# Kernel optimization log

Hardware: AMD Instinct MI355X
Metric: run time of the kernel (lower is better)

Reference implementation:

```python
import jax, jax.numpy as jnp
import numpy as np

VOCAB, EMB = 5000, 300
UNITS = [256, 512, 256]  # two return_sequences layers + final return-last layer
DENSE = 64


def lstm_layer(x, W, U, b, return_seq):
    """Keras-style LSTM with activation='relu', recurrent_activation='sigmoid'.
    x: [B,T,D]; W: [D,4u]; U: [u,4u]; b: [4u]. Gate order: i, f, c, o."""
    B = x.shape[0]
    u = U.shape[0]
    xg = jnp.einsum('btd,dg->btg', x, W) + b  # precompute input projections [B,T,4u]

    def step(carry, xg_t):
        h, c = carry
        g = xg_t + h @ U
        i, f, cc, o = jnp.split(g, 4, axis=-1)
        i = jax.nn.sigmoid(i)
        f = jax.nn.sigmoid(f)
        o = jax.nn.sigmoid(o)
        c = f * c + i * jax.nn.relu(cc)
        h = o * jax.nn.relu(c)
        return (h, c), h

    h0 = jnp.zeros((B, u), x.dtype)
    (hT, _), hs = jax.lax.scan(step, (h0, h0), jnp.swapaxes(xg, 0, 1))
    return jnp.swapaxes(hs, 0, 1) if return_seq else hT


def setup_inputs() -> dict:
    key = jax.random.key(0)
    ks = iter(jax.random.split(key, 16))
    s = 0.05  # small init keeps relu-LSTM numerically stable
    inp = {
        'tokens': jax.random.randint(next(ks), (128, 512), 0, VOCAB, dtype=jnp.int32),
        'emb': jax.random.normal(next(ks), (VOCAB, EMB), jnp.float32) * s,
    }
    d = EMB
    for li, u in enumerate(UNITS):
        inp[f'W{li}'] = jax.random.normal(next(ks), (d, 4 * u), jnp.float32) * s
        inp[f'U{li}'] = jax.random.normal(next(ks), (u, 4 * u), jnp.float32) * s
        inp[f'b{li}'] = jnp.zeros((4 * u,), jnp.float32)
        d = u
    inp['Wd'] = jax.random.normal(next(ks), (UNITS[-1], DENSE), jnp.float32) * s
    inp['bd'] = jnp.zeros((DENSE,), jnp.float32)
    inp['Wc'] = jax.random.normal(next(ks), (DENSE, 1), jnp.float32) * s
    inp['bc'] = jnp.zeros((1,), jnp.float32)
    return inp


def reference(tokens, emb, W0, U0, b0, W1, U1, b1, W2, U2, b2, Wd, bd, Wc, bc):
    x = emb[tokens]                                   # [B,T,300]
    x = lstm_layer(x, W0, U0, b0, return_seq=True)    # [B,T,256]
    x = lstm_layer(x, W1, U1, b1, return_seq=True)    # [B,T,512]
    x = lstm_layer(x, W2, U2, b2, return_seq=False)   # [B,256]
    x = jax.nn.relu(x @ Wd + bd)                      # [B,64]
    return jax.nn.sigmoid(x @ Wc + bc)                # [B,1]
```

## Files before the change

### kernel.cpp

```cpp
#include <hip/hip_runtime.h>
#include <cstdint>
#include <cstddef>

#define BATCH  128
#define SEQT   512
#define EMB_D  300
#define VOCABN 5000
#define KP0    320
#define NU0    256
#define NU1    512
#define NU2    256
#define NDENSE 64
#define RING   32
#define LIM    (1 << 19)

typedef unsigned short ushortT;
typedef unsigned long long ull;
typedef __attribute__((ext_vector_type(8))) short bf16x8;
typedef __attribute__((ext_vector_type(8))) unsigned short u16x8;
typedef __attribute__((ext_vector_type(4))) unsigned short u16x4;
typedef __attribute__((ext_vector_type(4))) float f32x4;

#define AGT __HIP_MEMORY_SCOPE_AGENT

static __device__ __forceinline__ unsigned short f2bf(float x) {
    union { float f; unsigned u; } v; v.f = x;
    const unsigned r = v.u + 0x7FFFu + ((v.u >> 16) & 1u);
    return (unsigned short)(r >> 16);
}
static __device__ __forceinline__ float bf2f(unsigned short b) {
    union { unsigned u; float f; } v; v.u = ((unsigned)b) << 16;
    return v.f;
}
static __device__ __forceinline__ float sigmoidf_(float x) {
    return 1.f / (1.f + __expf(-x));
}
static __device__ __forceinline__ unsigned ald(const unsigned* p) {
    return __hip_atomic_load((unsigned*)p, __ATOMIC_RELAXED, AGT);
}
static __device__ __forceinline__ void ast(unsigned* p, unsigned v) {
    __hip_atomic_store(p, v, __ATOMIC_RELAXED, AGT);
}
static __device__ __forceinline__ void ld16c(u16x8* d, const void* p) {
    asm volatile("global_load_dwordx4 %0, %1, off sc0 sc1"
                 : "=&v"(*d) : "v"(p) : "memory");
}
static __device__ __forceinline__ void ld8c(u16x4* d, const void* p) {
    asm volatile("global_load_dwordx2 %0, %1, off sc0 sc1"
                 : "=&v"(*d) : "v"(p) : "memory");
}
static __device__ __forceinline__ void st4c(void* p, unsigned v) {
    asm volatile("global_store_dword %0, %1, off sc0 sc1"
                 :: "v"(p), "v"(v) : "memory");
}
static __device__ __forceinline__ void wait0() {
    asm volatile("s_waitcnt vmcnt(0)" ::: "memory");
    __builtin_amdgcn_sched_barrier(0);
}
static __device__ __forceinline__ void wait2() {
    asm volatile("s_waitcnt vmcnt(2)" ::: "memory");
    __builtin_amdgcn_sched_barrier(0);
}

__global__ __launch_bounds__(256) void convert_WT(
    const float* __restrict__ W, ushortT* __restrict__ WbfT,
    int K, int NG, int KP, int total)
{
    for (int idx = blockIdx.x * 256 + threadIdx.x; idx < total; idx += gridDim.x * 256) {
        const int m = idx / KP, k = idx - m * KP;
        WbfT[idx] = (k < K) ? f2bf(W[(size_t)k * NG + m]) : (ushortT)0;
    }
}
__global__ __launch_bounds__(256) void convert_emb(
    const float* __restrict__ emb, ushortT* __restrict__ embbf)
{
    const int total = VOCABN * KP0;
    for (int idx = blockIdx.x * 256 + threadIdx.x; idx < total; idx += gridDim.x * 256) {
        const int v = idx / KP0, k = idx - v * KP0;
        embbf[idx] = (k < EMB_D) ? f2bf(emb[(size_t)v * EMB_D + k]) : (ushortT)0;
    }
}

__global__ __launch_bounds__(256) void gemm_xg0(
    const ushortT* __restrict__ embbf,
    const int*   __restrict__ tokens,
    const ushortT* __restrict__ W0T,
    const float* __restrict__ bias,
    ushortT* __restrict__ xg0)
{
    __shared__ ushortT Wl[128][32];
    __shared__ ushortT Xl[128][32];
    __shared__ int tokL[128];

    const int tid = threadIdx.x;
    const int t   = blockIdx.x;
    const int m0  = blockIdx.y * 128;
    const int wv  = tid >> 6;
    const int lane = tid & 63;
    const int lo  = lane & 15;
    const int hi  = lane >> 4;

    if (tid < 128) tokL[tid] = tokens[tid * SEQT + t];
    __syncthreads();

    f32x4 acc[2][8];
    #pragma unroll
    for (int s = 0; s < 2; ++s)
        #pragma unroll
        for (int n = 0; n < 8; ++n)
            acc[s][n] = f32x4{0.f, 0.f, 0.f, 0.f};

    for (int k0 = 0; k0 < KP0; k0 += 32) {
        #pragma unroll
        for (int it = 0; it < 2; ++it) {
            const int idx = tid + it * 256;
            const int row = idx >> 2, gq = idx & 3;
            const int gs  = gq ^ ((row >> 1) & 3);
            *(u16x8*)&Wl[row][gs * 8] =
                *(const u16x8*)(W0T + (size_t)(m0 + row) * KP0 + k0 + gq * 8);
            *(u16x8*)&Xl[row][gs * 8] =
                *(const u16x8*)(embbf + (size_t)tokL[row] * KP0 + k0 + gq * 8);
        }
        __syncthreads();

        bf16x8 bfr[8];
        #pragma unroll
        for (int n = 0; n < 8; ++n) {
            const int row = n * 16 + lo;
            bfr[n] = *(const bf16x8*)&Xl[row][(hi ^ ((row >> 1) & 3)) * 8];
        }
        #pragma unroll
        for (int s = 0; s < 2; ++s) {
            const int row = wv * 32 + s * 16 + lo;
            const bf16x8 a = *(const bf16x8*)&Wl[row][(hi ^ ((row >> 1) & 3)) * 8];
            #pragma unroll
            for (int n = 0; n < 8; ++n)
                acc[s][n] = __builtin_amdgcn_mfma_f32_16x16x32_bf16(a, bfr[n], acc[s][n], 0, 0, 0);
        }
        __syncthreads();
    }

    #pragma unroll
    for (int s = 0; s < 2; ++s)
        #pragma unroll
        for (int j = 0; j < 4; ++j) {
            const int m = m0 + wv * 32 + s * 16 + hi * 4 + j;
            const float bi = bias[m];
            #pragma unroll
            for (int n = 0; n < 8; ++n)
                xg0[(((size_t)t * 8 + n) * 1024 + m) * 16 + lo] = f2bf(acc[s][n][j] + bi);
        }
}

template<int U_, bool XATOMIC, int XTSH, int XPH>
__device__ void rec_role(
    int rid,
    const float* __restrict__ Umat,
    const ushortT* __restrict__ xgring, int xmask,
    ushortT* __restrict__ hring,
    unsigned* Fown,
    unsigned* Xown,
    unsigned* Xguard, int nGd,
    char* smem)
{
    constexpr int NGu = 4 * U_;
    constexpr int WPG = U_ / 64;
    constexpr int NWF = WPG * 4;
    constexpr int KT  = U_ / 32;
    constexpr int GR  = U_ / 8;
    constexpr int NLD = (16 * GR) / 256;

    ushortT* hstage = (ushortT*)smem;

    const int tid = threadIdx.x, w = tid >> 6, lane = tid & 63;
    const int lo = lane & 15, hi = lane >> 4;
    const int grp = rid & 7, wgj = rid >> 3;
    const int b0 = grp * 16, J = wgj * 64;
    const int jcol = J + w * 16 + lo;
    const size_t S = (size_t)128 * U_;

    bf16x8 bfr[4][KT];
    #pragma unroll
    for (int g = 0; g < 4; ++g)
        #pragma unroll
        for (int kt = 0; kt < KT; ++kt) {
            const float* up = Umat + (size_t)(kt * 32 + hi * 8) * NGu + g * U_ + jcol;
            bf16x8 v;
            #pragma unroll
            for (int i = 0; i < 8; ++i) v[i] = (short)f2bf(up[(size_t)i * NGu]);
            bfr[g][kt] = v;
        }

    float creg[4] = {0.f, 0.f, 0.f, 0.f};

    if (XATOMIC) {
        if (w == 0) {
            int guard = 0; bool ok;
            do {
                bool pred = true;
                if (lane < 4) {
                    const int mt = (lane * U_ + J) >> XTSH;
                    pred = ((int)ald(&Xown[(mt * XPH) * 16]) >= 1);
                }
                ok = __all(pred);
                if (!ok) __builtin_amdgcn_s_sleep(2);
            } while (!ok && ++guard < LIM);
        }
        __syncthreads();
    }
    u16x4 xnext[4];
    {
        const size_t xb = (size_t)grp * NGu;
        #pragma unroll
        for (int g = 0; g < 4; ++g) {
            const ushortT* ap = xgring + (xb + g * U_ + jcol) * 16 + hi * 4;
            if (XATOMIC) ld8c(&xnext[g], ap);
            else         xnext[g] = *(const u16x4*)ap;
        }
        if (XATOMIC) wait0();
    }

    for (int t = 0; t < SEQT; ++t) {
        if (w == 0) {
            int guard = 0; bool ok;
            do {
                bool pred = true;
                if (t > 0 && lane < NWF)
                    pred = ((int)ald(&Fown[(grp * NWF + lane) * 16]) >= t);
                if (XATOMIC && t + 1 < SEQT && lane >= 40 && lane < 44) {
                    const int mt = ((lane - 40) * U_ + J) >> XTSH;
                    const int fi = mt * XPH + ((t + 1) & (XPH - 1));
                    pred = pred && ((int)ald(&Xown[fi * 16]) >= t + 2);
                }
                for (int i = lane; i < nGd; i += 64)
                    pred = pred && ((int)ald(&Xguard[i * 16]) >= t - (RING - 1));
                ok = __all(pred);
                if (!ok) __builtin_amdgcn_s_sleep(1);
            } while (!ok && ++guard < LIM);
        }
        __syncthreads();

        u16x4 xcur[4];
        #pragma unroll
        for (int g = 0; g < 4; ++g) xcur[g] = xnext[g];

        u16x8 hr[NLD];
        if (t > 0) {
            const ushortT* hsrc = hring + (size_t)((t - 1) & (RING - 1)) * S;
            #pragma unroll
            for (int q = 0; q < NLD; ++q) {
                const int i = tid + q * 256;
                const int row = i / GR, gi = i - row * GR;
                ld16c(&hr[q], hsrc + (size_t)(b0 + row) * U_ + gi * 8);
            }
            wait0();
            #pragma unroll
            for (int q = 0; q < NLD; ++q) {
                const int i = tid + q * 256;
                const int row = i / GR, gi = i - row * GR;
                *(u16x8*)&hstage[(row * GR + (gi ^ (row & 7))) * 8] = hr[q];
            }
        }
        if (t + 1 < SEQT) {
            const size_t xb = (size_t)(((t + 1) & xmask) * 8 + grp) * NGu;
            #pragma unroll
            for (int g = 0; g < 4; ++g) {
                const ushortT* ap = xgring + (xb + g * U_ + jcol) * 16 + hi * 4;
                if (XATOMIC) ld8c(&xnext[g], ap);
                else         xnext[g] = *(const u16x4*)ap;
            }
        }
        __syncthreads();

        f32x4 acc[4];
        #pragma unroll
        for (int g = 0; g < 4; ++g) acc[g] = f32x4{0.f, 0.f, 0.f, 0.f};
        if (t > 0) {
            #pragma unroll
            for (int kt = 0; kt < KT; ++kt) {
                const int gs = (kt * 4 + hi) ^ (lo & 7);
                const bf16x8 a = *(const bf16x8*)&hstage[(lo * GR + gs) * 8];
                #pragma unroll
                for (int g = 0; g < 4; ++g)
                    acc[g] = __builtin_amdgcn_mfma_f32_16x16x32_bf16(a, bfr[g][kt], acc[g], 0, 0, 0);
            }
        }

        ushortT* hwr = hring + (size_t)(t & (RING - 1)) * S;
        unsigned own[4], oth[4];
        #pragma unroll
        for (int r = 0; r < 4; ++r) {
            const float i_ = sigmoidf_(acc[0][r] + bf2f(xcur[0][r]));
            const float f_ = sigmoidf_(acc[1][r] + bf2f(xcur[1][r]));
            const float cc = fmaxf(acc[2][r] + bf2f(xcur[2][r]), 0.f);
            const float o_ = sigmoidf_(acc[3][r] + bf2f(xcur[3][r]));
            creg[r] = f_ * creg[r] + i_ * cc;
            own[r] = (unsigned)f2bf(o_ * fmaxf(creg[r], 0.f));
        }
        #pragma unroll
        for (int r = 0; r < 4; ++r)
            oth[r] = (unsigned)__shfl_xor((int)own[r], 1);
        {
            const int odd = lo & 1;
            const int rb = odd ? 2 : 0;
            const int je = jcol - odd;
            #pragma unroll
            for (int q = 0; q < 2; ++q) {
                const int r = rb + q;
                const unsigned pk = odd ? (oth[r] | (own[r] << 16))
                                        : (own[r] | (oth[r] << 16));
                st4c(&hwr[(size_t)(b0 + hi * 4 + r) * U_ + je], pk);
            }
        }
        wait0();
        if (lane == 0)
            ast(&Fown[(grp * NWF + wgj * 4 + w) * 16], (unsigned)(t + 1));
    }
}

template<int MC, int NGATES, int KP, int P>
__device__ void worker_role(
    int mtile, int phase,
    const ushortT* __restrict__ WT,
    const float* __restrict__ bias,
    const ushortT* __restrict__ hring,
    ushortT* __restrict__ xgring,
    unsigned* Fup, int nUp,
    unsigned* Fguard, int nGd,
    unsigned* Xrel,
    char* smem)
{
    constexpr int GR2 = KP / 8;
    constexpr int NIT = KP / 32;
    constexpr int WR  = MC / 4;
    constexpr int MT  = WR / 16;
    ushortT* Wl = (ushortT*)smem;
    ushortT* Xl = (ushortT*)(smem + (size_t)MC * KP * 2);

    const int tid = threadIdx.x, w = tid >> 6, lane = tid & 63;
    const int lo = lane & 15, hi = lane >> 4;
    const int m0 = mtile * MC;
    const int row = tid >> 1, gq0 = (tid & 1) * 2;
    const int gs0 = gq0 ^ ((row >> 1) & 3);
    const int gs1 = (gq0 + 1) ^ ((row >> 1) & 3);

    for (int i = tid; i < MC * GR2; i += 256) {
        const int r_ = i / GR2, gi = i - r_ * GR2;
        const int gs = gi ^ (r_ & 7);
        *(u16x8*)&Wl[(r_ * GR2 + gs) * 8] =
            *(const u16x8*)(WT + (size_t)(m0 + r_) * KP + gi * 8);
    }
    float bv[MT][4];
    #pragma unroll
    for (int mt = 0; mt < MT; ++mt)
        #pragma unroll
        for (int j = 0; j < 4; ++j)
            bv[mt][j] = bias[m0 + w * WR + mt * 16 + hi * 4 + j];
    __syncthreads();

    for (int t = phase; t < SEQT; t += P) {
        if (w == 0) {
            int guard = 0; bool ok;
            do {
                bool pred = true;
                for (int i = lane; i < nUp; i += 64)
                    pred = pred && ((int)ald(&Fup[i * 16]) >= t + 1);
                for (int i = lane; i < nGd; i += 64)
                    pred = pred && ((int)ald(&Fguard[i * 16]) >= t - (RING - 1));
                ok = __all(pred);
                if (!ok) __builtin_amdgcn_s_sleep(32);
            } while (!ok && ++guard < LIM);
        }
        __syncthreads();

        const ushortT* hslab = hring + (size_t)(t & (RING - 1)) * 128 * KP;

        f32x4 acc[MT][8];
        #pragma unroll
        for (int mt = 0; mt < MT; ++mt)
            #pragma unroll
            for (int nn = 0; nn < 8; ++nn) acc[mt][nn] = f32x4{0.f, 0.f, 0.f, 0.f};

        u16x8 Ra0, Ra1, Rb0, Rb1;
        ld16c(&Ra0, hslab + (size_t)row * KP + gq0 * 8);
        ld16c(&Ra1, hslab + (size_t)row * KP + (gq0 + 1) * 8);
        #pragma unroll
        for (int it = 0; it < NIT; ++it) {
            const bool even = ((it & 1) == 0);
            if (it + 1 < NIT) {
                const ushortT* np = hslab + (size_t)row * KP + (it + 1) * 32;
                if (even) { ld16c(&Rb0, np + gq0 * 8); ld16c(&Rb1, np + (gq0 + 1) * 8); }
                else      { ld16c(&Ra0, np + gq0 * 8); ld16c(&Ra1, np + (gq0 + 1) * 8); }
                wait2();
            } else {
                wait0();
            }
            ushortT* Xc = Xl + (it & 1) * (128 * 32);
            *(u16x8*)&Xc[row * 32 + gs0 * 8] = even ? Ra0 : Rb0;
            *(u16x8*)&Xc[row * 32 + gs1 * 8] = even ? Ra1 : Rb1;
            __syncthreads();
            #pragma unroll
            for (int mt = 0; mt < MT; ++mt) {
                const int arow = w * WR + mt * 16 + lo;
                const int gsa = (it * 4 + hi) ^ (arow & 7);
                const bf16x8 a = *(const bf16x8*)&Wl[(arow * GR2 + gsa) * 8];
                #pragma unroll
                for (int nn = 0; nn < 8; ++nn) {
                    const int brow = nn * 16 + lo;
                    const bf16x8 b = *(const bf16x8*)&Xc[brow * 32 + (hi ^ ((brow >> 1) & 3)) * 8];
                    acc[mt][nn] = __builtin_amdgcn_mfma_f32_16x16x32_bf16(a, b, acc[mt][nn], 0, 0, 0);
                }
            }
            __syncthreads();
        }

        const size_t slab = (size_t)(t & (RING - 1)) * 8;
        #pragma unroll
        for (int mt = 0; mt < MT; ++mt) {
            #pragma unroll
            for (int nn = 0; nn < 8; ++nn) {
                const int b = nn * 16 + lo;
                unsigned own[4], oth[4];
                #pragma unroll
                for (int j = 0; j < 4; ++j)
                    own[j] = (unsigned)f2bf(acc[mt][nn][j] + bv[mt][j]);
                #pragma unroll
                for (int j = 0; j < 4; ++j)
                    oth[j] = (unsigned)__shfl_xor((int)own[j], 1);
                const int odd = lo & 1;
                const int jb = odd ? 2 : 0;
                const int be = (b & 15) - odd;
                #pragma unroll
                for (int q = 0; q < 2; ++q) {
                    const int j = jb + q;
                    const int m = m0 + w * WR + mt * 16 + hi * 4 + j;
                    const unsigned pk = odd ? (oth[j] | (own[j] << 16))
                                            : (own[j] | (oth[j] << 16));
                    st4c(&xgring[((slab + nn) * NGATES + m) * 16 + be], pk);
                }
            }
        }
        wait0();
        __syncthreads();
        if (tid == 0)
            ast(Xrel, (unsigned)(t + 1));
    }
}

struct MegaArgs {
    const float *U0, *U1, *U2;
    const ushortT *W1T, *W2T;
    const float *b1, *b2;
    const ushortT* xg0;
    ushortT *xg1, *xg2;
    ushortT *h0r, *h1r, *h2r;
    unsigned *F0, *F1, *F2, *X1, *X2;
};

__global__ __launch_bounds__(256, 1) void mega(MegaArgs A)
{
    extern __shared__ char smem[];
    const int bid = blockIdx.x;
    if (bid < 32) {
        rec_role<NU0, false, 1, 1>(bid, A.U0, A.xg0, 511, A.h0r, A.F0,
                                   nullptr, A.X1, 64, smem);
    } else if (bid < 96) {
        rec_role<NU1, true, 8, 8>(bid - 32, A.U1, A.xg1, RING - 1, A.h1r, A.F1,
                                  A.X1, A.X2, 32, smem);
    } else if (bid < 128) {
        rec_role<NU2, true, 7, 4>(bid - 96, A.U2, A.xg2, RING - 1, A.h2r, A.F2,
                                  A.X2, nullptr, 0, smem);
    } else if (bid < 192) {
        const int wid = bid - 128;
        const int mt = wid & 7, ph = wid >> 3;
        worker_role<256, 2048, 256, 8>(mt, ph, A.W1T, A.b1, A.h0r, A.xg1,
                                       A.F0, 128, A.F1, 256, A.X1 + (mt * 8 + ph) * 16, smem);
    } else {
        const int wid = bid - 192;
        const int mt = wid & 7, ph = wid >> 3;
        worker_role<128, 1024, 512, 4>(mt, ph, A.W2T, A.b2, A.h1r, A.xg2,
                                       A.F1, 256, A.F2, 128, A.X2 + (mt * 4 + ph) * 16, smem);
    }
}

__global__ __launch_bounds__(64) void head_kernel(
    const ushortT* __restrict__ h2,
    const float* __restrict__ Wd,
    const float* __restrict__ bd,
    const float* __restrict__ Wc,
    const float* __restrict__ bc,
    float* __restrict__ out)
{
    const int b = blockIdx.x;
    const int j = threadIdx.x;
    float a = bd[j];
    const ushortT* hrow = h2 + (size_t)b * NU2;
    #pragma unroll 4
    for (int k = 0; k < NU2; ++k)
        a += bf2f(hrow[k]) * Wd[(size_t)k * NDENSE + j];
    a = fmaxf(a, 0.f) * Wc[j];
    #pragma unroll
    for (int off = 32; off > 0; off >>= 1)
        a += __shfl_down(a, off);
    if (j == 0)
        out[b] = 1.f / (1.f + expf(-(a + bc[0])));
}

extern "C" void kernel_launch(void* const* d_in, const int* in_sizes, int n_in,
                              void* d_out, int out_size, void* d_ws, size_t ws_size,
                              hipStream_t stream)
{
    const int*   tokens = (const int*)  d_in[0];
    const float* emb    = (const float*)d_in[1];
    const float* W0     = (const float*)d_in[2];
    const float* Ur0    = (const float*)d_in[3];
    const float* b0v    = (const float*)d_in[4];
    const float* W1     = (const float*)d_in[5];
    const float* Ur1    = (const float*)d_in[6];
    const float* b1v    = (const float*)d_in[7];
    const float* W2     = (const float*)d_in[8];
    const float* Ur2    = (const float*)d_in[9];
    const float* b2v    = (const float*)d_in[10];
    const float* Wd     = (const float*)d_in[11];
    const float* bd     = (const float*)d_in[12];
    const float* Wc     = (const float*)d_in[13];
    const float* bc     = (const float*)d_in[14];
    float* out = (float*)d_out;

    char* p = (char*)d_ws;
    auto alloc = [&](size_t bytes) -> char* {
        char* q = p; p += (bytes + 255) & ~(size_t)255; return q;
    };
    ushortT* xg0   = (ushortT*)alloc((size_t)SEQT * 8 * 1024 * 16 * 2);
    ushortT* xg1   = (ushortT*)alloc((size_t)RING * 8 * 2048 * 16 * 2);
    ushortT* xg2   = (ushortT*)alloc((size_t)RING * 8 * 1024 * 16 * 2);
    ushortT* h0r   = (ushortT*)alloc((size_t)RING * 128 * NU0 * 2);
    ushortT* h1r   = (ushortT*)alloc((size_t)RING * 128 * NU1 * 2);
    ushortT* h2r   = (ushortT*)alloc((size_t)RING * 128 * NU2 * 2);
    ushortT* W0T   = (ushortT*)alloc((size_t)1024 * KP0 * 2);
    ushortT* W1T   = (ushortT*)alloc((size_t)2048 * NU0 * 2);
    ushortT* W2T   = (ushortT*)alloc((size_t)1024 * NU1 * 2);
    ushortT* embbf = (ushortT*)alloc((size_t)VOCABN * KP0 * 2);
    unsigned* flg  = (unsigned*)alloc(65536);

    unsigned* F0 = flg;
    unsigned* F1 = F0 + 128 * 16;
    unsigned* F2 = F1 + 256 * 16;
    unsigned* X1 = F2 + 128 * 16;
    unsigned* X2 = X1 + 64 * 16;

    hipMemsetAsync(flg, 0, 65536, stream);

    convert_WT<<<512, 256, 0, stream>>>(W0, W0T, EMB_D, 1024, KP0, 1024 * KP0);
    convert_WT<<<512, 256, 0, stream>>>(W1, W1T, NU0, 2048, NU0, 2048 * NU0);
    convert_WT<<<512, 256, 0, stream>>>(W2, W2T, NU1, 1024, NU1, 1024 * NU1);
    convert_emb<<<1024, 256, 0, stream>>>(emb, embbf);

    gemm_xg0<<<dim3(SEQT, 8), 256, 0, stream>>>(embbf, tokens, W0T, b0v, xg0);

    MegaArgs A;
    A.U0 = Ur0; A.U1 = Ur1; A.U2 = Ur2;
    A.W1T = W1T; A.W2T = W2T;
    A.b1 = b1v; A.b2 = b2v;
    A.xg0 = xg0; A.xg1 = xg1; A.xg2 = xg2;
    A.h0r = h0r; A.h1r = h1r; A.h2r = h2r;
    A.F0 = F0; A.F1 = F1; A.F2 = F2; A.X1 = X1; A.X2 = X2;

    void* args[] = {&A};
    hipLaunchCooperativeKernel((void*)mega, dim3(224), dim3(256), args, 147456, stream);

    head_kernel<<<BATCH, 64, 0, stream>>>(h2r + (size_t)31 * 128 * NU2,
                                          Wd, bd, Wc, bc, out);
}
```

Baseline: 2.634 ms.

## Replace per-step flag handshakes with timestep-tagged data words in rings

Each hidden-state and gate-projection element is stored as a 32-bit word: the bf16 value in the low half and the timestep tag in the high half. Consumers poll the data they need until the tags match, so most per-wavefront and per-tile flag waits and the barrier after each publish are gone. Coarse guard flags, checked every 8 steps, remain only to keep producers from overrunning the ring, and the ring depth is halved to 16. The price is double the bytes for ring traffic, extra memsets to clear the tags, and a bounded spin that could hide correctness problems if the tag checks time out.

```diff
diff --git a/kernel.cpp b/kernel.cpp
--- a/kernel.cpp
+++ b/kernel.cpp
@@ -11,14 +11,14 @@
 #define NU1    512
 #define NU2    256
 #define NDENSE 64
-#define RING   32
-#define LIM    (1 << 19)
+#define RING   16
+#define LIM    8192
 
 typedef unsigned short ushortT;
-typedef unsigned long long ull;
 typedef __attribute__((ext_vector_type(8))) short bf16x8;
 typedef __attribute__((ext_vector_type(8))) unsigned short u16x8;
 typedef __attribute__((ext_vector_type(4))) unsigned short u16x4;
+typedef __attribute__((ext_vector_type(4))) unsigned u32x4;
 typedef __attribute__((ext_vector_type(4))) float f32x4;
 
 #define AGT __HIP_MEMORY_SCOPE_AGENT
@@ -41,12 +41,8 @@
 static __device__ __forceinline__ void ast(unsigned* p, unsigned v) {
     __hip_atomic_store(p, v, __ATOMIC_RELAXED, AGT);
 }
-static __device__ __forceinline__ void ld16c(u16x8* d, const void* p) {
+static __device__ __forceinline__ void ld4u(u32x4* d, const void* p) {
     asm volatile("global_load_dwordx4 %0, %1, off sc0 sc1"
-                 : "=&v"(*d) : "v"(p) : "memory");
-}
-static __device__ __forceinline__ void ld8c(u16x4* d, const void* p) {
-    asm volatile("global_load_dwordx2 %0, %1, off sc0 sc1"
                  : "=&v"(*d) : "v"(p) : "memory");
 }
 static __device__ __forceinline__ void st4c(void* p, unsigned v) {
@@ -55,10 +51,6 @@
 }
 static __device__ __forceinline__ void wait0() {
     asm volatile("s_waitcnt vmcnt(0)" ::: "memory");
-    __builtin_amdgcn_sched_barrier(0);
-}
-static __device__ __forceinline__ void wait2() {
-    asm volatile("s_waitcnt vmcnt(2)" ::: "memory");
     __builtin_amdgcn_sched_barrier(0);
 }
 
@@ -123,11 +115,11 @@
         }
         __syncthreads();
 
-        bf16x8 bfr[8];
+        bf16x8 xfr[8];
         #pragma unroll
         for (int n = 0; n < 8; ++n) {
             const int row = n * 16 + lo;
-            bfr[n] = *(const bf16x8*)&Xl[row][(hi ^ ((row >> 1) & 3)) * 8];
+            xfr[n] = *(const bf16x8*)&Xl[row][(hi ^ ((row >> 1) & 3)) * 8];
         }
         #pragma unroll
         for (int s = 0; s < 2; ++s) {
@@ -135,7 +127,7 @@
             const bf16x8 a = *(const bf16x8*)&Wl[row][(hi ^ ((row >> 1) & 3)) * 8];
             #pragma unroll
             for (int n = 0; n < 8; ++n)
-                acc[s][n] = __builtin_amdgcn_mfma_f32_16x16x32_bf16(a, bfr[n], acc[s][n], 0, 0, 0);
+                acc[s][n] = __builtin_amdgcn_mfma_f32_16x16x32_bf16(a, xfr[n], acc[s][n], 0, 0, 0);
         }
         __syncthreads();
     }
@@ -152,23 +144,22 @@
         }
 }
 
-template<int U_, bool XATOMIC, int XTSH, int XPH>
+template<int U_, bool XTAG, int MARG>
 __device__ void rec_role(
     int rid,
     const float* __restrict__ Umat,
-    const ushortT* __restrict__ xgring, int xmask,
-    ushortT* __restrict__ hring,
-    unsigned* Fown,
-    unsigned* Xown,
-    unsigned* Xguard, int nGd,
+    const void* __restrict__ xgsrc, int xmask,
+    unsigned* __restrict__ hring,
+    unsigned* Fguard, int nGd,
+    unsigned* Fpub,
     char* smem)
 {
     constexpr int NGu = 4 * U_;
-    constexpr int WPG = U_ / 64;
-    constexpr int NWF = WPG * 4;
     constexpr int KT  = U_ / 32;
     constexpr int GR  = U_ / 8;
-    constexpr int NLD = (16 * GR) / 256;
+    constexpr int TPT = U_ / 16;
+    constexpr int NV  = TPT / 4;
+    constexpr int NGR = TPT / 8;
 
     ushortT* hstage = (ushortT*)smem;
 
@@ -177,6 +168,8 @@
     const int grp = rid & 7, wgj = rid >> 3;
     const int b0 = grp * 16, J = wgj * 64;
     const int jcol = J + w * 16 + lo;
+    const int srow = tid >> 4;
+    const int scol = (tid & 15) * TPT;
     const size_t S = (size_t)128 * U_;
 
     bf16x8 bfr[4][KT];
@@ -193,82 +186,97 @@
 
     float creg[4] = {0.f, 0.f, 0.f, 0.f};
 
-    if (XATOMIC) {
-        if (w == 0) {
-            int guard = 0; bool ok;
+    for (int t = 0; t < SEQT; ++t) {
+        if (nGd && (t & 7) == 0 && w == 0) {
+            int gd = 0; bool ok;
             do {
-                bool pred = true;
-                if (lane < 4) {
-                    const int mt = (lane * U_ + J) >> XTSH;
-                    pred = ((int)ald(&Xown[(mt * XPH) * 16]) >= 1);
-                }
-                ok = __all(pred);
-                if (!ok) __builtin_amdgcn_s_sleep(2);
-            } while (!ok && ++guard < LIM);
-        }
-        __syncthreads();
-    }
-    u16x4 xnext[4];
-    {
-        const size_t xb = (size_t)grp * NGu;
-        #pragma unroll
-        for (int g = 0; g < 4; ++g) {
-            const ushortT* ap = xgring + (xb + g * U_ + jcol) * 16 + hi * 4;
-            if (XATOMIC) ld8c(&xnext[g], ap);
-            else         xnext[g] = *(const u16x4*)ap;
-        }
-        if (XATOMIC) wait0();
-    }
-
-    for (int t = 0; t < SEQT; ++t) {
-        if (w == 0) {
-            int guard = 0; bool ok;
-            do {
-                bool pred = true;
-                if (t > 0 && lane < NWF)
-                    pred = ((int)ald(&Fown[(grp * NWF + lane) * 16]) >= t);
-                if (XATOMIC && t + 1 < SEQT && lane >= 40 && lane < 44) {
-                    const int mt = ((lane - 40) * U_ + J) >> XTSH;
-                    const int fi = mt * XPH + ((t + 1) & (XPH - 1));
-                    pred = pred && ((int)ald(&Xown[fi * 16]) >= t + 2);
-                }
+                bool pr = true;
                 for (int i = lane; i < nGd; i += 64)
-                    pred = pred && ((int)ald(&Xguard[i * 16]) >= t - (RING - 1));
-                ok = __all(pred);
-                if (!ok) __builtin_amdgcn_s_sleep(1);
-            } while (!ok && ++guard < LIM);
-        }
-        __syncthreads();
-
-        u16x4 xcur[4];
-        #pragma unroll
-        for (int g = 0; g < 4; ++g) xcur[g] = xnext[g];
-
-        u16x8 hr[NLD];
+                    pr = pr && ((int)ald(&Fguard[i * 16]) >= t - MARG);
+                ok = __all(pr);
+                if (!ok) __builtin_amdgcn_s_sleep(8);
+            } while (!ok && ++gd < LIM);
+        }
+
+        u32x4 xw[4];
+        float xg[4][4];
+        if (XTAG) {
+            const unsigned* xb = (const unsigned*)xgsrc
+                + ((size_t)(t & xmask) * 8 + grp) * NGu * 16;
+            #pragma unroll
+            for (int g = 0; g < 4; ++g)
+                ld4u(&xw[g], xb + ((size_t)g * U_ + jcol) * 16 + hi * 4);
+        } else {
+            const ushortT* xb = (const ushortT*)xgsrc
+                + ((size_t)(t & xmask) * 8 + grp) * NGu * 16;
+            #pragma unroll
+            for (int g = 0; g < 4; ++g) {
+                const u16x4 v = *(const u16x4*)(xb + ((size_t)g * U_ + jcol) * 16 + hi * 4);
+                #pragma unroll
+                for (int e = 0; e < 4; ++e) xg[g][e] = bf2f(v[e]);
+            }
+        }
+        u32x4 hv[NV];
+        const unsigned* hp = nullptr;
         if (t > 0) {
-            const ushortT* hsrc = hring + (size_t)((t - 1) & (RING - 1)) * S;
-            #pragma unroll
-            for (int q = 0; q < NLD; ++q) {
-                const int i = tid + q * 256;
-                const int row = i / GR, gi = i - row * GR;
-                ld16c(&hr[q], hsrc + (size_t)(b0 + row) * U_ + gi * 8);
-            }
-            wait0();
-            #pragma unroll
-            for (int q = 0; q < NLD; ++q) {
-                const int i = tid + q * 256;
-                const int row = i / GR, gi = i - row * GR;
-                *(u16x8*)&hstage[(row * GR + (gi ^ (row & 7))) * 8] = hr[q];
-            }
-        }
-        if (t + 1 < SEQT) {
-            const size_t xb = (size_t)(((t + 1) & xmask) * 8 + grp) * NGu;
-            #pragma unroll
-            for (int g = 0; g < 4; ++g) {
-                const ushortT* ap = xgring + (xb + g * U_ + jcol) * 16 + hi * 4;
-                if (XATOMIC) ld8c(&xnext[g], ap);
-                else         xnext[g] = *(const u16x4*)ap;
-            }
+            hp = hring + (size_t)((t - 1) & (RING - 1)) * S + (size_t)(b0 + srow) * U_ + scol;
+            #pragma unroll
+            for (int q = 0; q < NV; ++q) ld4u(&hv[q], hp + q * 4);
+        }
+        wait0();
+
+        if (t > 0) {
+            const unsigned exp = (unsigned)t;
+            int gd = 0;
+            for (;;) {
+                bool ok = true;
+                #pragma unroll
+                for (int q = 0; q < NV; ++q)
+                    #pragma unroll
+                    for (int e = 0; e < 4; ++e)
+                        ok = ok && ((hv[q][e] >> 16) == exp);
+                if (ok || ++gd >= LIM) break;
+                __builtin_amdgcn_s_sleep(1);
+                #pragma unroll
+                for (int q = 0; q < NV; ++q) ld4u(&hv[q], hp + q * 4);
+                wait0();
+            }
+            ushortT* hb = hstage + (size_t)(t & 1) * 16 * U_;
+            #pragma unroll
+            for (int gr = 0; gr < NGR; ++gr) {
+                u16x8 v;
+                #pragma unroll
+                for (int e = 0; e < 4; ++e) v[e]     = (ushortT)hv[gr * 2][e];
+                #pragma unroll
+                for (int e = 0; e < 4; ++e) v[4 + e] = (ushortT)hv[gr * 2 + 1][e];
+                const int gi = scol / 8 + gr;
+                *(u16x8*)&hb[(srow * GR + (gi ^ (srow & 7))) * 8] = v;
+            }
+        }
+        if (XTAG) {
+            const unsigned* xb = (const unsigned*)xgsrc
+                + ((size_t)(t & xmask) * 8 + grp) * NGu * 16;
+            const unsigned exp = (unsigned)(t + 1);
+            int gd = 0;
+            for (;;) {
+                bool ok = true;
+                #pragma unroll
+                for (int g = 0; g < 4; ++g)
+                    #pragma unroll
+                    for (int e = 0; e < 4; ++e)
+                        ok = ok && ((xw[g][e] >> 16) == exp);
+                if (ok || ++gd >= LIM) break;
+                __builtin_amdgcn_s_sleep(1);
+                #pragma unroll
+                for (int g = 0; g < 4; ++g)
+                    ld4u(&xw[g], xb + ((size_t)g * U_ + jcol) * 16 + hi * 4);
+                wait0();
+            }
+            #pragma unroll
+            for (int g = 0; g < 4; ++g)
+                #pragma unroll
+                for (int e = 0; e < 4; ++e)
+                    xg[g][e] = bf2f((ushortT)xw[g][e]);
         }
         __syncthreads();
 
@@ -276,62 +284,47 @@
         #pragma unroll
         for (int g = 0; g < 4; ++g) acc[g] = f32x4{0.f, 0.f, 0.f, 0.f};
         if (t > 0) {
+            const ushortT* hb = hstage + (size_t)(t & 1) * 16 * U_;
             #pragma unroll
             for (int kt = 0; kt < KT; ++kt) {
                 const int gs = (kt * 4 + hi) ^ (lo & 7);
-                const bf16x8 a = *(const bf16x8*)&hstage[(lo * GR + gs) * 8];
+                const bf16x8 a = *(const bf16x8*)&hb[(lo * GR + gs) * 8];
                 #pragma unroll
                 for (int g = 0; g < 4; ++g)
                     acc[g] = __builtin_amdgcn_mfma_f32_16x16x32_bf16(a, bfr[g][kt], acc[g], 0, 0, 0);
             }
         }
 
-        ushortT* hwr = hring + (size_t)(t & (RING - 1)) * S;
-        unsigned own[4], oth[4];
+        unsigned* hw = hring + (size_t)(t & (RING - 1)) * S;
+        const unsigned tg = ((unsigned)(t + 1)) << 16;
         #pragma unroll
         for (int r = 0; r < 4; ++r) {
-            const float i_ = sigmoidf_(acc[0][r] + bf2f(xcur[0][r]));
-            const float f_ = sigmoidf_(acc[1][r] + bf2f(xcur[1][r]));
-            const float cc = fmaxf(acc[2][r] + bf2f(xcur[2][r]), 0.f);
-            const float o_ = sigmoidf_(acc[3][r] + bf2f(xcur[3][r]));
+            const float i_ = sigmoidf_(acc[0][r] + xg[0][r]);
+            const float f_ = sigmoidf_(acc[1][r] + xg[1][r]);
+            const float cc = fmaxf(acc[2][r] + xg[2][r], 0.f);
+            const float o_ = sigmoidf_(acc[3][r] + xg[3][r]);
             creg[r] = f_ * creg[r] + i_ * cc;
-            own[r] = (unsigned)f2bf(o_ * fmaxf(creg[r], 0.f));
-        }
-        #pragma unroll
-        for (int r = 0; r < 4; ++r)
-            oth[r] = (unsigned)__shfl_xor((int)own[r], 1);
-        {
-            const int odd = lo & 1;
-            const int rb = odd ? 2 : 0;
-            const int je = jcol - odd;
-            #pragma unroll
-            for (int q = 0; q < 2; ++q) {
-                const int r = rb + q;
-                const unsigned pk = odd ? (oth[r] | (own[r] << 16))
-                                        : (own[r] | (oth[r] << 16));
-                st4c(&hwr[(size_t)(b0 + hi * 4 + r) * U_ + je], pk);
-            }
-        }
-        wait0();
-        if (lane == 0)
-            ast(&Fown[(grp * NWF + wgj * 4 + w) * 16], (unsigned)(t + 1));
-    }
-}
-
-template<int MC, int NGATES, int KP, int P>
+            const float hn = o_ * fmaxf(creg[r], 0.f);
+            st4c(&hw[(size_t)(b0 + hi * 4 + r) * U_ + jcol], tg | (unsigned)f2bf(hn));
+        }
+        if (Fpub && (t & 7) == 7 && tid == 0)
+            ast(Fpub, (unsigned)(t + 1));
+    }
+}
+
+template<int MC, int NG, int KP, int P>
 __device__ void worker_role(
     int mtile, int phase,
     const ushortT* __restrict__ WT,
     const float* __restrict__ bias,
-    const ushortT* __restrict__ hring,
-    ushortT* __restrict__ xgring,
-    unsigned* Fup, int nUp,
+    const unsigned* __restrict__ hring,
+    unsigned* __restrict__ xgring,
     unsigned* Fguard, int nGd,
-    unsigned* Xrel,
+    unsigned* Fpub,
     char* smem)
 {
-    constexpr int GR2 = KP / 8;
-    constexpr int NIT = KP / 32;
+    constexpr int GRW = KP / 8;
+    constexpr int NC  = KP / 32;
     constexpr int WR  = MC / 4;
     constexpr int MT  = WR / 16;
     ushortT* Wl = (ushortT*)smem;
@@ -340,14 +333,13 @@
     const int tid = threadIdx.x, w = tid >> 6, lane = tid & 63;
     const int lo = lane & 15, hi = lane >> 4;
     const int m0 = mtile * MC;
-    const int row = tid >> 1, gq0 = (tid & 1) * 2;
-    const int gs0 = gq0 ^ ((row >> 1) & 3);
-    const int gs1 = (gq0 + 1) ^ ((row >> 1) & 3);
-
-    for (int i = tid; i < MC * GR2; i += 256) {
-        const int r_ = i / GR2, gi = i - r_ * GR2;
-        const int gs = gi ^ (r_ & 7);
-        *(u16x8*)&Wl[(r_ * GR2 + gs) * 8] =
+    const int crow = tid >> 1;
+    const int ccol = (tid & 1) * 16;
+    const int cg0  = ccol / 8;
+
+    for (int i = tid; i < MC * GRW; i += 256) {
+        const int r_ = i / GRW, gi = i - r_ * GRW;
+        *(u16x8*)&Wl[(r_ * GRW + (gi ^ (r_ & 7))) * 8] =
             *(const u16x8*)(WT + (size_t)(m0 + r_) * KP + gi * 8);
     }
     float bv[MT][4];
@@ -360,20 +352,18 @@
 
     for (int t = phase; t < SEQT; t += P) {
         if (w == 0) {
-            int guard = 0; bool ok;
+            int gd = 0; bool ok;
             do {
-                bool pred = true;
-                for (int i = lane; i < nUp; i += 64)
-                    pred = pred && ((int)ald(&Fup[i * 16]) >= t + 1);
+                bool pr = true;
                 for (int i = lane; i < nGd; i += 64)
-                    pred = pred && ((int)ald(&Fguard[i * 16]) >= t - (RING - 1));
-                ok = __all(pred);
-                if (!ok) __builtin_amdgcn_s_sleep(32);
-            } while (!ok && ++guard < LIM);
-        }
-        __syncthreads();
-
-        const ushortT* hslab = hring + (size_t)(t & (RING - 1)) * 128 * KP;
+                    pr = pr && ((int)ald(&Fguard[i * 16]) >= t - 15);
+                ok = __all(pr);
+                if (!ok) __builtin_amdgcn_s_sleep(16);
+            } while (!ok && ++gd < LIM);
+        }
+
+        const unsigned* hslab = hring + (size_t)(t & (RING - 1)) * 128 * KP;
+        const unsigned exp = (unsigned)(t + 1);
 
         f32x4 acc[MT][8];
         #pragma unroll
@@ -381,69 +371,65 @@
             #pragma unroll
             for (int nn = 0; nn < 8; ++nn) acc[mt][nn] = f32x4{0.f, 0.f, 0.f, 0.f};
 
-        u16x8 Ra0, Ra1, Rb0, Rb1;
-        ld16c(&Ra0, hslab + (size_t)row * KP + gq0 * 8);
-        ld16c(&Ra1, hslab + (size_t)row * KP + (gq0 + 1) * 8);
-        #pragma unroll
-        for (int it = 0; it < NIT; ++it) {
-            const bool even = ((it & 1) == 0);
-            if (it + 1 < NIT) {
-                const ushortT* np = hslab + (size_t)row * KP + (it + 1) * 32;
-                if (even) { ld16c(&Rb0, np + gq0 * 8); ld16c(&Rb1, np + (gq0 + 1) * 8); }
-                else      { ld16c(&Ra0, np + gq0 * 8); ld16c(&Ra1, np + (gq0 + 1) * 8); }
-                wait2();
-            } else {
+        for (int kc = 0; kc < NC; ++kc) {
+            u32x4 cw[4];
+            const unsigned* cp = hslab + (size_t)crow * KP + kc * 32 + ccol;
+            #pragma unroll
+            for (int q = 0; q < 4; ++q) ld4u(&cw[q], cp + q * 4);
+            wait0();
+            int gd = 0;
+            for (;;) {
+                bool ok = true;
+                #pragma unroll
+                for (int q = 0; q < 4; ++q)
+                    #pragma unroll
+                    for (int e = 0; e < 4; ++e)
+                        ok = ok && ((cw[q][e] >> 16) == exp);
+                if (ok || ++gd >= LIM) break;
+                __builtin_amdgcn_s_sleep(2);
+                #pragma unroll
+                for (int q = 0; q < 4; ++q) ld4u(&cw[q], cp + q * 4);
                 wait0();
             }
-            ushortT* Xc = Xl + (it & 1) * (128 * 32);
-            *(u16x8*)&Xc[row * 32 + gs0 * 8] = even ? Ra0 : Rb0;
-            *(u16x8*)&Xc[row * 32 + gs1 * 8] = even ? Ra1 : Rb1;
+            #pragma unroll
+            for (int gq2 = 0; gq2 < 2; ++gq2) {
+                u16x8 v;
+                #pragma unroll
+                for (int e = 0; e < 4; ++e) v[e]     = (ushortT)cw[gq2 * 2][e];
+                #pragma unroll
+                for (int e = 0; e < 4; ++e) v[4 + e] = (ushortT)cw[gq2 * 2 + 1][e];
+                const int g4 = cg0 + gq2;
+                *(u16x8*)&Xl[crow * 32 + (g4 ^ ((crow >> 1) & 3)) * 8] = v;
+            }
             __syncthreads();
             #pragma unroll
             for (int mt = 0; mt < MT; ++mt) {
                 const int arow = w * WR + mt * 16 + lo;
-                const int gsa = (it * 4 + hi) ^ (arow & 7);
-                const bf16x8 a = *(const bf16x8*)&Wl[(arow * GR2 + gsa) * 8];
+                const int gsa = (kc * 4 + hi) ^ (arow & 7);
+                const bf16x8 a = *(const bf16x8*)&Wl[(arow * GRW + gsa) * 8];
                 #pragma unroll
                 for (int nn = 0; nn < 8; ++nn) {
                     const int brow = nn * 16 + lo;
-                    const bf16x8 b = *(const bf16x8*)&Xc[brow * 32 + (hi ^ ((brow >> 1) & 3)) * 8];
+                    const bf16x8 b = *(const bf16x8*)&Xl[brow * 32 + (hi ^ ((brow >> 1) & 3)) * 8];
                     acc[mt][nn] = __builtin_amdgcn_mfma_f32_16x16x32_bf16(a, b, acc[mt][nn], 0, 0, 0);
                 }
             }
             __syncthreads();
         }
 
-        const size_t slab = (size_t)(t & (RING - 1)) * 8;
-        #pragma unroll
-        for (int mt = 0; mt < MT; ++mt) {
-            #pragma unroll
-            for (int nn = 0; nn < 8; ++nn) {
-                const int b = nn * 16 + lo;
-                unsigned own[4], oth[4];
-                #pragma unroll
-                for (int j = 0; j < 4; ++j)
-                    own[j] = (unsigned)f2bf(acc[mt][nn][j] + bv[mt][j]);
-                #pragma unroll
-                for (int j = 0; j < 4; ++j)
-                    oth[j] = (unsigned)__shfl_xor((int)own[j], 1);
-                const int odd = lo & 1;
-                const int jb = odd ? 2 : 0;
-                const int be = (b & 15) - odd;
-                #pragma unroll
-                for (int q = 0; q < 2; ++q) {
-                    const int j = jb + q;
+        unsigned* xb = xgring + (size_t)(t & (RING - 1)) * 8 * NG * 16;
+        const unsigned tg = ((unsigned)(t + 1)) << 16;
+        #pragma unroll
+        for (int mt = 0; mt < MT; ++mt)
+            #pragma unroll
+            for (int nn = 0; nn < 8; ++nn)
+                #pragma unroll
+                for (int j = 0; j < 4; ++j) {
                     const int m = m0 + w * WR + mt * 16 + hi * 4 + j;
-                    const unsigned pk = odd ? (oth[j] | (own[j] << 16))
-                                            : (own[j] | (oth[j] << 16));
-                    st4c(&xgring[((slab + nn) * NGATES + m) * 16 + be], pk);
+                    st4c(xb + ((size_t)nn * NG + m) * 16 + lo,
+                         tg | (unsigned)f2bf(acc[mt][nn][j] + bv[mt][j]));
                 }
-            }
-        }
-        wait0();
-        __syncthreads();
-        if (tid == 0)
-            ast(Xrel, (unsigned)(t + 1));
+        if (tid == 0) ast(Fpub, (unsigned)(t + 1));
     }
 }
 
@@ -452,9 +438,9 @@
     const ushortT *W1T, *W2T;
     const float *b1, *b2;
     const ushortT* xg0;
-    ushortT *xg1, *xg2;
-    ushortT *h0r, *h1r, *h2r;
-    unsigned *F0, *F1, *F2, *X1, *X2;
+    unsigned *xg1, *xg2;
+    unsigned *h0r, *h1r, *h2r;
+    unsigned *FL1, *FL2, *FG1, *FG2;
 };
 
 __global__ __launch_bounds__(256, 1) void mega(MegaArgs A)
@@ -462,29 +448,29 @@
     extern __shared__ char smem[];
     const int bid = blockIdx.x;
     if (bid < 32) {
-        rec_role<NU0, false, 1, 1>(bid, A.U0, A.xg0, 511, A.h0r, A.F0,
-                                   nullptr, A.X1, 64, smem);
+        rec_role<NU0, false, 15>(bid, A.U0, A.xg0, 511, A.h0r,
+                                 A.FG1, 64, nullptr, smem);
     } else if (bid < 96) {
-        rec_role<NU1, true, 8, 8>(bid - 32, A.U1, A.xg1, RING - 1, A.h1r, A.F1,
-                                  A.X1, A.X2, 32, smem);
+        rec_role<NU1, true, 11>(bid - 32, A.U1, A.xg1, RING - 1, A.h1r,
+                                A.FG2, 32, A.FL1 + (bid - 32) * 16, smem);
     } else if (bid < 128) {
-        rec_role<NU2, true, 7, 4>(bid - 96, A.U2, A.xg2, RING - 1, A.h2r, A.F2,
-                                  A.X2, nullptr, 0, smem);
+        rec_role<NU2, true, 15>(bid - 96, A.U2, A.xg2, RING - 1, A.h2r,
+                                nullptr, 0, A.FL2 + (bid - 96) * 16, smem);
     } else if (bid < 192) {
         const int wid = bid - 128;
         const int mt = wid & 7, ph = wid >> 3;
         worker_role<256, 2048, 256, 8>(mt, ph, A.W1T, A.b1, A.h0r, A.xg1,
-                                       A.F0, 128, A.F1, 256, A.X1 + (mt * 8 + ph) * 16, smem);
+                                       A.FL1, 64, A.FG1 + wid * 16, smem);
     } else {
         const int wid = bid - 192;
         const int mt = wid & 7, ph = wid >> 3;
         worker_role<128, 1024, 512, 4>(mt, ph, A.W2T, A.b2, A.h1r, A.xg2,
-                                       A.F1, 256, A.F2, 128, A.X2 + (mt * 4 + ph) * 16, smem);
+                                       A.FL2, 32, A.FG2 + wid * 16, smem);
     }
 }
 
 __global__ __launch_bounds__(64) void head_kernel(
-    const ushortT* __restrict__ h2,
+    const unsigned* __restrict__ h2r,
     const float* __restrict__ Wd,
     const float* __restrict__ bd,
     const float* __restrict__ Wc,
@@ -493,11 +479,11 @@
 {
     const int b = blockIdx.x;
     const int j = threadIdx.x;
+    const unsigned* hrow = h2r + ((size_t)15 * 128 + b) * NU2;
     float a = bd[j];
-    const ushortT* hrow = h2 + (size_t)b * NU2;
     #pragma unroll 4
     for (int k = 0; k < NU2; ++k)
-        a += bf2f(hrow[k]) * Wd[(size_t)k * NDENSE + j];
+        a += bf2f((ushortT)hrow[k]) * Wd[(size_t)k * NDENSE + j];
     a = fmaxf(a, 0.f) * Wc[j];
     #pragma unroll
     for (int off = 32; off > 0; off >>= 1)
@@ -531,25 +517,29 @@
     auto alloc = [&](size_t bytes) -> char* {
         char* q = p; p += (bytes + 255) & ~(size_t)255; return q;
     };
-    ushortT* xg0   = (ushortT*)alloc((size_t)SEQT * 8 * 1024 * 16 * 2);
-    ushortT* xg1   = (ushortT*)alloc((size_t)RING * 8 * 2048 * 16 * 2);
-    ushortT* xg2   = (ushortT*)alloc((size_t)RING * 8 * 1024 * 16 * 2);
-    ushortT* h0r   = (ushortT*)alloc((size_t)RING * 128 * NU0 * 2);
-    ushortT* h1r   = (ushortT*)alloc((size_t)RING * 128 * NU1 * 2);
-    ushortT* h2r   = (ushortT*)alloc((size_t)RING * 128 * NU2 * 2);
-    ushortT* W0T   = (ushortT*)alloc((size_t)1024 * KP0 * 2);
-    ushortT* W1T   = (ushortT*)alloc((size_t)2048 * NU0 * 2);
-    ushortT* W2T   = (ushortT*)alloc((size_t)1024 * NU1 * 2);
-    ushortT* embbf = (ushortT*)alloc((size_t)VOCABN * KP0 * 2);
-    unsigned* flg  = (unsigned*)alloc(65536);
-
-    unsigned* F0 = flg;
-    unsigned* F1 = F0 + 128 * 16;
-    unsigned* F2 = F1 + 256 * 16;
-    unsigned* X1 = F2 + 128 * 16;
-    unsigned* X2 = X1 + 64 * 16;
-
-    hipMemsetAsync(flg, 0, 65536, stream);
+    ushortT*  xg0  = (ushortT*)alloc((size_t)SEQT * 8 * 1024 * 16 * 2);
+    unsigned* xg1  = (unsigned*)alloc((size_t)RING * 8 * 2048 * 16 * 4);
+    unsigned* xg2  = (unsigned*)alloc((size_t)RING * 8 * 1024 * 16 * 4);
+    unsigned* h0r  = (unsigned*)alloc((size_t)RING * 128 * NU0 * 4);
+    unsigned* h1r  = (unsigned*)alloc((size_t)RING * 128 * NU1 * 4);
+    unsigned* h2r  = (unsigned*)alloc((size_t)RING * 128 * NU2 * 4);
+    ushortT*  W0T  = (ushortT*)alloc((size_t)1024 * KP0 * 2);
+    ushortT*  W1T  = (ushortT*)alloc((size_t)2048 * NU0 * 2);
+    ushortT*  W2T  = (ushortT*)alloc((size_t)1024 * NU1 * 2);
+    ushortT*  embbf= (ushortT*)alloc((size_t)VOCABN * KP0 * 2);
+    unsigned* flg  = (unsigned*)alloc(16384);
+
+    unsigned* FL1 = flg;
+    unsigned* FL2 = flg + 64 * 16;
+    unsigned* FG1 = flg + 96 * 16;
+    unsigned* FG2 = flg + 160 * 16;
+
+    hipMemsetAsync(xg1, 0, (size_t)RING * 8 * 2048 * 16 * 4, stream);
+    hipMemsetAsync(xg2, 0, (size_t)RING * 8 * 1024 * 16 * 4, stream);
+    hipMemsetAsync(h0r, 0, (size_t)RING * 128 * NU0 * 4, stream);
+    hipMemsetAsync(h1r, 0, (size_t)RING * 128 * NU1 * 4, stream);
+    hipMemsetAsync(h2r, 0, (size_t)RING * 128 * NU2 * 4, stream);
+    hipMemsetAsync(flg, 0, 16384, stream);
 
     convert_WT<<<512, 256, 0, stream>>>(W0, W0T, EMB_D, 1024, KP0, 1024 * KP0);
     convert_WT<<<512, 256, 0, stream>>>(W1, W1T, NU0, 2048, NU0, 2048 * NU0);
@@ -564,11 +554,10 @@
     A.b1 = b1v; A.b2 = b2v;
     A.xg0 = xg0; A.xg1 = xg1; A.xg2 = xg2;
     A.h0r = h0r; A.h1r = h1r; A.h2r = h2r;
-    A.F0 = F0; A.F1 = F1; A.F2 = F2; A.X1 = X1; A.X2 = X2;
+    A.FL1 = FL1; A.FL2 = FL2; A.FG1 = FG1; A.FG2 = FG2;
 
     void* args[] = {&A};
-    hipLaunchCooperativeKernel((void*)mega, dim3(224), dim3(256), args, 147456, stream);
-
-    head_kernel<<<BATCH, 64, 0, stream>>>(h2r + (size_t)31 * 128 * NU2,
-                                          Wd, bd, Wc, bc, out);
-}
+    hipLaunchCooperativeKernel((void*)mega, dim3(224), dim3(256), args, 139264, stream);
+
+    head_kernel<<<BATCH, 64, 0, stream>>>(h2r, Wd, bd, Wc, bc, out);
+}
```

Result: slower. 2.919 ms (+10.8%).
